# Kernel optimization log

Measured on AMD Instinct MI355X. Metric: run time of the kernel, lower is better.

## Reference

```python
import jax, jax.numpy as jnp
import numpy as np

PAD_MAG = 1e12
EPS = 1e-7  # matches prev_step.add_(1e-07) in the torch code


def setup_inputs() -> dict:
    key = jax.random.key(0)
    k1, k2, k3, k4 = jax.random.split(key, 4)
    B, txt_T, mel_T, n_mel = 16, 320, 2000, 80
    mu_logvar = jax.random.normal(k1, (B, txt_T, 2 * n_mel), dtype=jnp.float32)
    melspec = jax.random.normal(k2, (B, n_mel, mel_T), dtype=jnp.float32)
    text_lengths = jax.random.randint(k3, (B,), txt_T // 2, txt_T + 1).astype(jnp.int32)
    mel_lengths = jax.random.randint(k4, (B,), mel_T // 2, mel_T + 1).astype(jnp.int32)
    return {"mu_logvar": mu_logvar, "melspec": melspec,
            "text_lengths": text_lengths, "mel_lengths": mel_lengths}


def _log_prob_matrix(mu_logvar, melspec):
    # exponential[b,j,t] = -0.5 * mean_c( (x[b,t,c]-mu[b,j,c])^2 / exp(logvar) + logvar )
    # avoiding the [B,txt_T,mel_T,n_mel] broadcast the torch code materializes.
    n_mel = melspec.shape[1]
    mu = mu_logvar[:, :, :n_mel]          # [B, txt_T, n_mel]
    logvar = mu_logvar[:, :, n_mel:]      # [B, txt_T, n_mel]
    x = jnp.swapaxes(melspec, 1, 2)       # [B, mel_T, n_mel]
    inv_var = jnp.exp(-logvar)
    xx = jnp.einsum('btc,bjc->bjt', x * x, inv_var)
    xm = jnp.einsum('btc,bjc->bjt', x, mu * inv_var)
    mm = jnp.sum(mu * mu * inv_var + logvar, axis=2)  # [B, txt_T]
    return (-0.5 / n_mel) * (xx - 2.0 * xm + mm[:, :, None])  # [B, txt_T, mel_T]


def _forward_dp(log_prob, text_lengths, mel_lengths):
    # monotonic alignment forward algorithm (logsumexp DP over mel frames)
    B, txt_T, mel_T = log_prob.shape
    # carry = log_alpha column of size txt_T+1 (row 0 is the -inf pad row)
    init = jnp.full((B, txt_T + 1), -PAD_MAG, log_prob.dtype)
    init = init.at[:, 1].set(log_prob[:, 0, 0])

    def step(a, lp):  # a: [B, txt_T+1], lp: [B, txt_T]
        prev = jnp.stack([a[:, 1:], a[:, :-1]], axis=-1) + EPS
        tail = jax.nn.logsumexp(prev, axis=-1) + lp      # [B, txt_T]
        a_new = jnp.concatenate(
            [jnp.full((B, 1), -PAD_MAG, a.dtype), tail], axis=1)
        return a_new, tail

    lps = jnp.moveaxis(log_prob[:, :, 1:], 2, 0)         # [mel_T-1, B, txt_T]
    _, tails = jax.lax.scan(step, init, lps)             # [mel_T-1, B, txt_T]
    log_alpha = jnp.concatenate([init[None, :, 1:], tails], axis=0)  # [mel_T, B, txt_T]
    log_alpha = jnp.moveaxis(log_alpha, 0, 2)            # [B, txt_T, mel_T]

    bidx = jnp.arange(B)
    alpha_last = log_alpha[bidx, text_lengths - 1, mel_lengths - 1]
    alpha_last = alpha_last / mel_lengths.astype(log_alpha.dtype)
    return -jnp.mean(alpha_last)


def reference(mu_logvar, melspec, text_lengths, mel_lengths):
    log_prob = _log_prob_matrix(mu_logvar, melspec)
    mdn_loss = _forward_dp(log_prob, text_lengths, mel_lengths)
    return (mdn_loss, log_prob)
```

## Files before the change

kernel.cpp:

```cpp
#include <hip/hip_runtime.h>

#define BATCH 16
#define TXT   320
#define NMELC 80
#define MELT  2000
#define PADM  1.0e12f
#define EPSC  1e-7f
#define L2E   1.4426950408889634f
#define LN2   0.6931471805599453f
#define EPSL2 1.4426950e-7f

__global__ __launch_bounds__(256) void lp_kernel(
    const float* __restrict__ mlv,
    const float* __restrict__ ms,
    float* __restrict__ out_lp)
{
    __shared__ float Gt[16][64];
    __shared__ float Ft[16][256];
    __shared__ float bias_s[64];
    __shared__ float bias_p[256];

    const int b   = blockIdx.z;
    const int j0  = blockIdx.y * 64;
    const int t0  = blockIdx.x * 256;
    const int tid = threadIdx.x;
    const float s = -0.00625f;

    const float* mlv_b = mlv + (size_t)b * TXT * 160;
    const float* ms_b  = ms  + (size_t)b * NMELC * MELT;

    {
        const int jj = tid >> 2;
        const int q  = tid & 3;
        const float* p = mlv_b + (size_t)(j0 + jj) * 160 + q * 20;
        float part = 0.f;
        #pragma unroll
        for (int c = 0; c < 20; ++c) {
            float mu = p[c];
            float lv = p[c + 80];
            float iv = __expf(-lv);
            part += mu * mu * iv + lv;
        }
        bias_p[tid] = part;
    }
    __syncthreads();
    if (tid < 64) {
        float v = bias_p[tid * 4] + bias_p[tid * 4 + 1] +
                  bias_p[tid * 4 + 2] + bias_p[tid * 4 + 3];
        bias_s[tid] = s * v;
    }

    float acc[8][8];
    #pragma unroll
    for (int i = 0; i < 8; ++i)
        #pragma unroll
        for (int k = 0; k < 8; ++k) acc[i][k] = 0.f;

    const int jg = tid >> 5;
    const int tg = tid & 31;

    for (int kc = 0; kc < 10; ++kc) {
        const int c0 = kc * 8;
        __syncthreads();
        #pragma unroll
        for (int i = 0; i < 2; ++i) {
            int f   = tid + i * 256;
            int cr  = f >> 6;
            int col = f & 63;
            float mu = mlv_b[(size_t)(j0 + col) * 160 + (c0 + cr)];
            float lv = mlv_b[(size_t)(j0 + col) * 160 + (80 + c0 + cr)];
            float iv = __expf(-lv);
            Gt[cr][col]     = s * iv;
            Gt[cr + 8][col] = -2.f * s * mu * iv;
        }
        #pragma unroll
        for (int i = 0; i < 2; ++i) {
            int f   = tid + i * 256;
            int row = f >> 6;
            int c4  = f & 63;
            int t   = t0 + c4 * 4;
            float4 v = (t + 3 < MELT)
                ? *(const float4*)&ms_b[(size_t)(c0 + row) * MELT + t]
                : make_float4(0.f, 0.f, 0.f, 0.f);
            *(float4*)&Ft[row][c4 * 4] =
                make_float4(v.x * v.x, v.y * v.y, v.z * v.z, v.w * v.w);
            *(float4*)&Ft[row + 8][c4 * 4] = v;
        }
        __syncthreads();
        #pragma unroll
        for (int k = 0; k < 16; ++k) {
            float4 g0 = *(const float4*)&Gt[k][jg * 8];
            float4 g1 = *(const float4*)&Gt[k][jg * 8 + 4];
            float4 f0 = *(const float4*)&Ft[k][tg * 8];
            float4 f1 = *(const float4*)&Ft[k][tg * 8 + 4];
            float ga[8] = {g0.x, g0.y, g0.z, g0.w, g1.x, g1.y, g1.z, g1.w};
            float fa[8] = {f0.x, f0.y, f0.z, f0.w, f1.x, f1.y, f1.z, f1.w};
            #pragma unroll
            for (int ji = 0; ji < 8; ++ji)
                #pragma unroll
                for (int ti = 0; ti < 8; ++ti)
                    acc[ji][ti] = fmaf(ga[ji], fa[ti], acc[ji][ti]);
        }
    }

    #pragma unroll
    for (int ji = 0; ji < 8; ++ji) {
        int j = j0 + jg * 8 + ji;
        float bs = bias_s[jg * 8 + ji];
        float* orow = out_lp + (size_t)(b * TXT + j) * MELT;
        #pragma unroll
        for (int ti = 0; ti < 8; ++ti) {
            int t = t0 + tg * 8 + ti;
            if (t < MELT) orow[t] = acc[ji][ti] + bs;
        }
    }
}

__device__ __forceinline__ float dpp_shr1(float x) {
    return __int_as_float(__builtin_amdgcn_update_dpp(
        0, __float_as_int(x), 0x138 , 0xF, 0xF, false));
}

__global__ __launch_bounds__(192, 1) void dp_kernel(
    const float* __restrict__ lp,
    const int* __restrict__ tlen,
    const int* __restrict__ mlen,
    float* __restrict__ res,
    float* __restrict__ out0)
{
    __shared__ float bnd[2][2056];
    __shared__ int   prog[2];

    const int b    = blockIdx.x;
    const int tid  = threadIdx.x;
    const int w    = tid >> 6;
    const int l    = tid & 63;
    const int tend = mlen[b] - 1;
    const int tl   = tlen[b];

    if (tid < 2) prog[tid] = 0;

    int j0c = 2 * tid; if (j0c > 318) j0c = 318;
    const float* r0 = lp + (size_t)(b * TXT + j0c) * MELT;
    const float* r1 = r0 + MELT;

    float A1 = (tid == 0) ? lp[(size_t)b * TXT * MELT] * L2E : -PADM;
    float A2 = -PADM;
    float A1F = A1, A2F = A2;

    if (l == 63 && w < 2) bnd[w][0] = -PADM;
    __syncthreads();

    if (w == 2 && tl < 257) return;

    float ptA2 = -PADM, ptB2 = -PADM;
    const bool is0     = (l == 0);
    const bool isPub   = (l == 63) && (w < 2);
    const bool hasRing = (w > 0);
    int seen = 0;

    const int imax = tend + 63;

    float PA[16], PB[16], PC[16];
    #pragma unroll
    for (int q = 0; q < 8; ++q) { PA[2*q] = r0[1 + q - l]; PA[2*q+1] = r1[1 + q - l]; }
    #pragma unroll
    for (int q = 0; q < 8; ++q) { PB[2*q] = r0[9 + q - l]; PB[2*q+1] = r1[9 + q - l]; }
    #pragma unroll
    for (int q = 0; q < 16; ++q) PA[q] = fmaf(PA[q], L2E, EPSL2);

    const float* p0 = r0 + 17 - l;
    const float* p1 = r1 + 17 - l;

#define RING_RD(BQ_, T0_)                                                    \
    {                                                                        \
        float4 r0_ = *(const float4*)&bnd[w - 1][T0_];                       \
        float4 r1_ = *(const float4*)&bnd[w - 1][(T0_) + 4];                 \
        BQ_[0]=r0_.x; BQ_[1]=r0_.y; BQ_[2]=r0_.z; BQ_[3]=r0_.w;              \
        BQ_[4]=r1_.x; BQ_[5]=r1_.y; BQ_[6]=r1_.z; BQ_[7]=r1_.w;              \
    }
#define RING_POLL(NEED_)                                                     \
    if (seen < (NEED_)) {                                                    \
        int tgt_ = (NEED_) + 32;                                             \
        if (tgt_ > tend - 1) tgt_ = tend - 1;                                \
        if (tgt_ < (NEED_)) tgt_ = (NEED_);                                  \
        volatile int* pv_ = &prog[w - 1];                                    \
        int v_ = *pv_;                                                       \
        while (v_ < tgt_) { __builtin_amdgcn_s_sleep(1); v_ = *pv_; }        \
        seen = v_;                                                           \
        __asm__ volatile("" ::: "memory");                                   \
    }

    float bqC[8];
    if (hasRing) {
        RING_POLL(7)
        RING_RD(bqC, 0)
    } else {
        #pragma unroll
        for (int q = 0; q < 8; ++q) bqC[q] = -PADM;
    }

#define STEP2(Pc_, q_, AQ_)                                                  \
    {                                                                        \
        float pt_ = is0 ? bqC[q_] : ptA2;                                    \
        float m1_ = fmaxf(A1, pt_);                                          \
        float d1_ = A1 - pt_;                                                \
        float e1_ = __builtin_amdgcn_exp2f(-fabsf(d1_));                     \
        float g1_ = __builtin_amdgcn_logf(1.0f + e1_);                       \
        float n1_ = m1_ + g1_ + Pc_[2 * q_];                                 \
        float m2_ = fmaxf(A2, A1);                                           \
        float d2_ = A2 - A1;                                                 \
        float e2_ = __builtin_amdgcn_exp2f(-fabsf(d2_));                     \
        float g2_ = __builtin_amdgcn_logf(1.0f + e2_);                       \
        float n2_ = m2_ + g2_ + Pc_[2 * q_ + 1];                             \
        float ns_ = dpp_shr1(n2_);                                           \
        ptA2 = ptB2; ptB2 = ns_;                                             \
        A1 = n1_; A2 = n2_; AQ_ = n2_;                                       \
    }

#define GROUP2_S(Pc_, Pm_, Pl_, I0_)                                         \
{                                                                            \
    float bqN[8];                                                            \
    if (hasRing) {                                                           \
        const int nt0_ = (I0_) + 7;                                          \
        RING_POLL(nt0_ + 7)                                                  \
        RING_RD(bqN, nt0_)                                                   \
    } else {                                                                 \
        _Pragma("unroll") for (int q_=0;q_<8;++q_) bqN[q_] = -PADM;          \
    }                                                                        \
    _Pragma("unroll") for (int q_=0;q_<8;++q_) {                             \
        Pl_[2*q_] = p0[q_]; Pl_[2*q_+1] = p1[q_];                            \
    }                                                                        \
    float aq2[8];                                                            \
    _Pragma("unroll")                                                        \
    for (int q_=0;q_<8;++q_) STEP2(Pc_, q_, aq2[q_])                         \
    if (isPub) {                                                             \
        const int t63_ = (I0_) - 63;                                         \
        if (t63_ >= 1) {                                                     \
            _Pragma("unroll") for (int q_=0;q_<8;++q_)                       \
                bnd[w][t63_ + q_] = aq2[q_];                                 \
        } else {                                                             \
            _Pragma("unroll") for (int q_=0;q_<8;++q_)                       \
                if (t63_ + q_ >= 1) bnd[w][t63_ + q_] = aq2[q_];             \
        }                                                                    \
        __asm__ volatile("" ::: "memory");          \
        int pgv_ = t63_ + 7;                                                 \
        if (pgv_ >= 1) prog[w] = pgv_;                                       \
    }                                                                        \
    p0 += 8; p1 += 8;                                                        \
    _Pragma("unroll") for (int q_=0;q_<16;++q_)                              \
        Pm_[q_] = fmaf(Pm_[q_], L2E, EPSL2);                                 \
    _Pragma("unroll") for (int q_=0;q_<8;++q_) bqC[q_] = bqN[q_];            \
}

#define GROUP2_T(Pc_, Pm_, Pl_, I0_)                                         \
{                                                                            \
    float bqN[8];                                                            \
    if (hasRing) {                                                           \
        const int nt0_ = (I0_) + 7;                                          \
        int need_ = nt0_ + 7; if (need_ > tend - 1) need_ = tend - 1;        \
        RING_POLL(need_)                                                     \
        const int rb_ = nt0_ > 2048 ? 2048 : nt0_;                           \
        RING_RD(bqN, rb_)                                                    \
    } else {                                                                 \
        _Pragma("unroll") for (int q_=0;q_<8;++q_) bqN[q_] = -PADM;          \
    }                                                                        \
    _Pragma("unroll") for (int q_=0;q_<8;++q_) {                             \
        int t_ = (I0_) + 16 + q_ - l;                                        \
        t_ = t_ < 0 ? 0 : (t_ > tend ? tend : t_);                           \
        Pl_[2*q_] = r0[t_]; Pl_[2*q_+1] = r1[t_];                            \
    }                                                                        \
    float aq2[8];                                                            \
    const int vt_ = (I0_) - l;                                               \
    _Pragma("unroll")                                                        \
    for (int q_=0;q_<8;++q_) {                                               \
        STEP2(Pc_, q_, aq2[q_])                                              \
        bool c_ = (vt_ + q_ == tend);                                        \
        A1F = c_ ? A1 : A1F;                                                 \
        A2F = c_ ? A2 : A2F;                                                 \
    }                                                                        \
    if (isPub) {                                                             \
        const int t63_ = (I0_) - 63;                                         \
        _Pragma("unroll") for (int q_=0;q_<8;++q_) {                         \
            int tq_ = t63_ + q_;                                             \
            if (tq_ >= 1 && tq_ <= tend) bnd[w][tq_] = aq2[q_];              \
        }                                                                    \
        __asm__ volatile("" ::: "memory");                                   \
        int pgv_ = t63_ + 7; if (pgv_ > tend) pgv_ = tend;                   \
        if (pgv_ >= 1) prog[w] = pgv_;                                       \
    }                                                                        \
    _Pragma("unroll") for (int q_=0;q_<16;++q_)                              \
        Pm_[q_] = fmaf(Pm_[q_], L2E, EPSL2);                                 \
    _Pragma("unroll") for (int q_=0;q_<8;++q_) bqC[q_] = bqN[q_];            \
}

    int i0 = 1;
    const int sEnd = tend - 23;
    int ph = 0;
    while (i0 <= sEnd) {
        GROUP2_S(PA, PB, PC, i0); i0 += 8;
        if (i0 > sEnd) { ph = 1; break; }
        GROUP2_S(PB, PC, PA, i0); i0 += 8;
        if (i0 > sEnd) { ph = 2; break; }
        GROUP2_S(PC, PA, PB, i0); i0 += 8;
    }
    if (ph == 1) {
        #pragma unroll
        for (int q = 0; q < 16; ++q) {
            float tmp = PA[q]; PA[q] = PB[q]; PB[q] = PC[q]; PC[q] = tmp;
        }
    } else if (ph == 2) {
        #pragma unroll
        for (int q = 0; q < 16; ++q) {
            float tmp = PA[q]; PA[q] = PC[q]; PC[q] = PB[q]; PB[q] = tmp;
        }
    }
    while (i0 <= imax) {
        GROUP2_T(PA, PB, PC, i0); i0 += 8;
        if (i0 > imax) break;
        GROUP2_T(PB, PC, PA, i0); i0 += 8;
        if (i0 > imax) break;
        GROUP2_T(PC, PA, PB, i0); i0 += 8;
    }

#undef GROUP2_S
#undef GROUP2_T
#undef STEP2
#undef RING_RD
#undef RING_POLL

    if (tid == ((tl - 1) >> 1)) {
        float Af = ((tl - 1) & 1) ? A2F : A1F;
        float v = Af * LN2 / (float)(tend + 1);
        if (res) res[b] = v;
        else     atomicAdd(out0, -v / (float)BATCH);
    }
}

__global__ void zero1_kernel(float* out0) { out0[0] = 0.f; }

__global__ void fin_kernel(const float* __restrict__ res, float* __restrict__ out0)
{
    int l = threadIdx.x;
    float v = (l < BATCH) ? res[l] : 0.f;
    #pragma unroll
    for (int off = 32; off; off >>= 1) v += __shfl_down(v, off);
    if (l == 0) out0[0] = -(v / (float)BATCH);
}

extern "C" void kernel_launch(void* const* d_in, const int* in_sizes, int n_in,
                              void* d_out, int out_size, void* d_ws, size_t ws_size,
                              hipStream_t stream)
{
    const float* mlv = (const float*)d_in[0];
    const float* ms  = (const float*)d_in[1];
    const int*   tl  = (const int*)d_in[2];
    const int*   ml  = (const int*)d_in[3];
    float* out    = (float*)d_out;
    float* out_lp = out + 1;

    bool res_ok = ws_size >= 64;
    float* res = res_ok ? (float*)d_ws : nullptr;

    dim3 gA(8, 5, 16);
    lp_kernel<<<gA, 256, 0, stream>>>(mlv, ms, out_lp);

    if (!res_ok) zero1_kernel<<<1, 1, 0, stream>>>(out);
    dp_kernel<<<BATCH, 192, 0, stream>>>(out_lp, tl, ml, res, out);
    if (res_ok) fin_kernel<<<1, 64, 0, stream>>>(res, out);
}
```

Baseline: 244.7 us.

## Precompute 4-step DP transition coefficients in parallel kernel, then run strided wavefront DP

New measurement: 937.8 us. 283% more time.

```diff
diff --git a/kernel.cpp b/kernel.cpp
--- a/kernel.cpp
+++ b/kernel.cpp
@@ -4,7 +4,9 @@
 #define TXT   320
 #define NMELC 80
 #define MELT  2000
+#define NW    504
 #define PADM  1.0e12f
+#define INF9  1.0e9f
 #define EPSC  1e-7f
 #define L2E   1.4426950408889634f
 #define LN2   0.6931471805599453f
@@ -116,12 +118,264 @@
     }
 }
 
+__device__ __forceinline__ float lse2l(float x, float y) {
+    float m = fmaxf(x, y);
+    float d = x - y;
+    float e = __builtin_amdgcn_exp2f(-fabsf(d));
+    return m + __builtin_amdgcn_logf(1.0f + e);
+}
+
+__global__ __launch_bounds__(320) void coeff_kernel(
+    const float* __restrict__ lp,
+    const int* __restrict__ mlen,
+    float* __restrict__ Cc)
+{
+    __shared__ float sl[320][65];
+
+    const int Wg  = blockIdx.x;
+    const int b   = blockIdx.y;
+    const int tid = threadIdx.x;
+    const int tend = mlen[b] - 1;
+
+    {
+        const int g  = tid >> 6;
+        const int tl_ = tid & 63;
+        const int t  = 64 * Wg + 1 + tl_;
+        for (int r = 0; r < 64; ++r) {
+            int j = g * 64 + r;
+            float v = (t < MELT) ? lp[((size_t)b * TXT + j) * MELT + t] : 0.f;
+            sl[j][tl_] = fmaf(v, L2E, EPSL2);
+        }
+    }
+    __syncthreads();
+
+    const int j = tid;
+    const int j1 = j >= 1 ? j - 1 : 0;
+    const int j2 = j >= 2 ? j - 2 : 0;
+    const int j3 = j >= 3 ? j - 3 : 0;
+
+    for (int wi = 0; wi < 16; ++wi) {
+        const int W = Wg * 16 + wi;
+        if (W >= NW) break;
+        const int col = 4 * wi;
+
+        float B0[5] = {0.f, -INF9, -INF9, -INF9, -INF9};
+        float B1[5] = {0.f, -INF9, -INF9, -INF9, -INF9};
+        float B2[5] = {0.f, -INF9, -INF9, -INF9, -INF9};
+        float B3[5] = {0.f, -INF9, -INF9, -INF9, -INF9};
+
+        if (4 * W + 1 <= tend) {
+            float p0 = sl[j][col], p1 = sl[j1][col], p2 = sl[j2][col], p3 = sl[j3][col];
+            B3[1] = p3 + lse2l(B3[1], 0.f);      B3[0] = p3 + B3[0];
+            B2[1] = p2 + lse2l(B2[1], B3[0] - p3);
+        }
+        {
+            float O0[5], O1[5], O2[5], O3[5];
+            #pragma unroll
+            for (int r = 0; r < 5; ++r) { O0[r]=0.f; O1[r]=0.f; O2[r]=0.f; O3[r]=0.f; }
+            #pragma unroll
+            for (int r = 0; r < 5; ++r) {
+                B0[r] = r==0?0.f:-INF9; B1[r] = r==0?0.f:-INF9;
+                B2[r] = r==0?0.f:-INF9; B3[r] = r==0?0.f:-INF9;
+            }
+            if (4 * W + 1 <= tend) {
+                float p0 = sl[j][col], p1 = sl[j1][col], p2 = sl[j2][col], p3 = sl[j3][col];
+                #pragma unroll
+                for (int r = 0; r < 5; ++r) { O0[r]=B0[r]; O1[r]=B1[r]; O2[r]=B2[r]; O3[r]=B3[r]; }
+                B0[0] = p0 + O0[0];  B0[1] = p0 + lse2l(O0[1], O1[0]);
+                B1[0] = p1 + O1[0];  B1[1] = p1 + lse2l(O1[1], O2[0]);
+                B2[0] = p2 + O2[0];  B2[1] = p2 + lse2l(O2[1], O3[0]);
+                B3[0] = p3 + O3[0];  B3[1] = p3 + lse2l(O3[1], 0.f);
+            }
+            if (4 * W + 2 <= tend) {
+                float p0 = sl[j][col+1], p1 = sl[j1][col+1], p2 = sl[j2][col+1];
+                #pragma unroll
+                for (int r = 0; r < 5; ++r) { O0[r]=B0[r]; O1[r]=B1[r]; O2[r]=B2[r]; O3[r]=B3[r]; }
+                B0[0] = p0 + O0[0];
+                B0[1] = p0 + lse2l(O0[1], O1[0]);
+                B0[2] = p0 + lse2l(O0[2], O1[1]);
+                B1[0] = p1 + O1[0];
+                B1[1] = p1 + lse2l(O1[1], O2[0]);
+                B1[2] = p1 + lse2l(O1[2], O2[1]);
+                B2[0] = p2 + O2[0];
+                B2[1] = p2 + lse2l(O2[1], O3[0]);
+                B2[2] = p2 + lse2l(O2[2], O3[1]);
+            }
+            if (4 * W + 3 <= tend) {
+                float p0 = sl[j][col+2], p1 = sl[j1][col+2];
+                #pragma unroll
+                for (int r = 0; r < 5; ++r) { O0[r]=B0[r]; O1[r]=B1[r]; O2[r]=B2[r]; }
+                B0[0] = p0 + O0[0];
+                B0[1] = p0 + lse2l(O0[1], O1[0]);
+                B0[2] = p0 + lse2l(O0[2], O1[1]);
+                B0[3] = p0 + lse2l(O0[3], O1[2]);
+                B1[0] = p1 + O1[0];
+                B1[1] = p1 + lse2l(O1[1], O2[0]);
+                B1[2] = p1 + lse2l(O1[2], O2[1]);
+                B1[3] = p1 + lse2l(O1[3], O2[2]);
+            }
+            if (4 * W + 4 <= tend) {
+                float p0 = sl[j][col+3];
+                #pragma unroll
+                for (int r = 0; r < 5; ++r) { O0[r]=B0[r]; O1[r]=B1[r]; }
+                B0[0] = p0 + O0[0];
+                B0[1] = p0 + lse2l(O0[1], O1[0]);
+                B0[2] = p0 + lse2l(O0[2], O1[1]);
+                B0[3] = p0 + lse2l(O0[3], O1[2]);
+                B0[4] = p0 + lse2l(O0[4], O1[3]);
+            }
+        }
+        if (j < 1) B0[1] = -INF9;
+        if (j < 2) B0[2] = -INF9;
+        if (j < 3) B0[3] = -INF9;
+        if (j < 4) B0[4] = -INF9;
+
+        float* cp = Cc + (((size_t)b * NW + W) * 5) * 320 + j;
+        cp[0]    = B0[0];
+        cp[320]  = B0[1];
+        cp[640]  = B0[2];
+        cp[960]  = B0[3];
+        cp[1280] = B0[4];
+    }
+}
+
 __device__ __forceinline__ float dpp_shr1(float x) {
     return __int_as_float(__builtin_amdgcn_update_dpp(
         0, __float_as_int(x), 0x138 , 0xF, 0xF, false));
 }
 
-__global__ __launch_bounds__(192, 1) void dp_kernel(
+__global__ __launch_bounds__(320, 1) void dp_kernel(
+    const float* __restrict__ Cc,
+    const float* __restrict__ lp,
+    const int* __restrict__ tlen,
+    const int* __restrict__ mlen,
+    float* __restrict__ res,
+    float* __restrict__ out0)
+{
+    __shared__ float bnd[4][NW][4];
+    __shared__ int   prog[4];
+
+    const int b    = blockIdx.x;
+    const int tid  = threadIdx.x;
+    const int w    = tid >> 6;
+    const int l    = tid & 63;
+    const int j    = tid;
+    const int tend = mlen[b] - 1;
+    const int tl   = tlen[b];
+    const int Wmax = (tend + 3) >> 2;
+
+    if (tid < 4) prog[tid] = 0;
+
+    float a  = (j == 0) ? lp[(size_t)b * TXT * MELT] * L2E : -PADM;
+    float aF = a;
+    if (l >= 60 && w < 4) bnd[w][0][l - 60] = a;
+    __syncthreads();
+
+    float H1 = -PADM, H2 = -PADM, H3 = -PADM, H4 = -PADM;
+    const bool hasRing = (w > 0);
+    int seen = -1;
+    const float* Cb = Cc + ((size_t)b * NW * 5) * 320 + j;
+    const int imax = Wmax - 1 + 63;
+
+    float CA[4][5], CB[4][5];
+    float RA[4][4], RB[4][4];
+    #pragma unroll
+    for (int q = 0; q < 4; ++q)
+        #pragma unroll
+        for (int k = 0; k < 4; ++k) { RA[q][k] = -PADM; RB[q][k] = -PADM; }
+
+#define CLAMPW(I_, OUT_) { int W_ = (I_) - l; W_ = W_ < 0 ? 0 : W_;          \
+    OUT_ = W_ > Wmax - 1 ? Wmax - 1 : W_; }
+
+#define POLLTO(TGT_) if (hasRing) {                                          \
+    int need_ = (TGT_); if (need_ > Wmax - 1) need_ = Wmax - 1;              \
+    if (seen < need_) {                                                      \
+        int t2_ = need_ + 16; if (t2_ > Wmax - 1) t2_ = Wmax - 1;            \
+        volatile int* pv_ = &prog[w - 1];                                    \
+        int v_ = *pv_;                                                       \
+        while (v_ < t2_) { __builtin_amdgcn_s_sleep(1); v_ = *pv_; }         \
+        seen = v_;                                                           \
+        __asm__ volatile("" ::: "memory");                                   \
+    } }
+
+#define LOADG(CX_, RX_, IB_) {                                               \
+    _Pragma("unroll")                                                        \
+    for (int q_ = 0; q_ < 4; ++q_) {                                         \
+        int We_; CLAMPW((IB_) + q_, We_)                                     \
+        const float* cp_ = Cb + (size_t)We_ * 1600;                          \
+        CX_[q_][0] = cp_[0];    CX_[q_][1] = cp_[320];                       \
+        CX_[q_][2] = cp_[640];  CX_[q_][3] = cp_[960];                       \
+        CX_[q_][4] = cp_[1280];                                              \
+        if (hasRing) {                                                       \
+            if (l < 1) RX_[q_][0] = bnd[w - 1][We_][3];                      \
+            if (l < 2) RX_[q_][1] = bnd[w - 1][We_][l + 2];                  \
+            if (l < 3) RX_[q_][2] = bnd[w - 1][We_][l + 1];                  \
+            if (l < 4) RX_[q_][3] = bnd[w - 1][We_][l];                      \
+        }                                                                    \
+    } }
+
+#define STEP(CQ_, RQ_, I_) {                                                 \
+    H4 = dpp_shr1(H3); H3 = dpp_shr1(H2); H2 = dpp_shr1(H1);                 \
+    H1 = dpp_shr1(a);                                                        \
+    float N1_ = (l >= 1) ? H1 : RQ_[0];                                      \
+    float N2_ = (l >= 2) ? H2 : RQ_[1];                                      \
+    float N3_ = (l >= 3) ? H3 : RQ_[2];                                      \
+    float N4_ = (l >= 4) ? H4 : RQ_[3];                                      \
+    float x0_ = a   + CQ_[0];                                                \
+    float x1_ = N1_ + CQ_[1];                                                \
+    float x2_ = N2_ + CQ_[2];                                                \
+    float x3_ = N3_ + CQ_[3];                                                \
+    float x4_ = N4_ + CQ_[4];                                                \
+    float m_ = fmaxf(fmaxf(fmaxf(x0_, x1_), fmaxf(x2_, x3_)), x4_);          \
+    float s_ = __builtin_amdgcn_exp2f(x0_ - m_)                              \
+             + __builtin_amdgcn_exp2f(x1_ - m_)                              \
+             + __builtin_amdgcn_exp2f(x2_ - m_)                              \
+             + __builtin_amdgcn_exp2f(x3_ - m_)                              \
+             + __builtin_amdgcn_exp2f(x4_ - m_);                             \
+    a = m_ + __builtin_amdgcn_logf(s_);                                      \
+    aF = ((I_) - l == Wmax - 1) ? a : aF;                                    \
+    if (l >= 60 && w < 4) {                                                  \
+        int Wp_ = (I_) - l + 1;                                              \
+        if (Wp_ >= 1 && Wp_ <= Wmax - 1) bnd[w][Wp_][l - 60] = a;            \
+    } }
+
+#define PHASE(CC_, RC_, CN_, RN_, I0_) {                                     \
+    POLLTO((I0_) + 7)                                                        \
+    LOADG(CN_, RN_, (I0_) + 4)                                               \
+    STEP(CC_[0], RC_[0], (I0_) + 0)                                          \
+    STEP(CC_[1], RC_[1], (I0_) + 1)                                          \
+    STEP(CC_[2], RC_[2], (I0_) + 2)                                          \
+    STEP(CC_[3], RC_[3], (I0_) + 3)                                          \
+    if (l == 63 && w < 4) {                                                  \
+        __asm__ volatile("s_waitcnt lgkmcnt(0)" ::: "memory");               \
+        int pv_ = (I0_) + 3 - 62;                                            \
+        if (pv_ > Wmax - 1) pv_ = Wmax - 1;                                  \
+        if (pv_ >= 0) prog[w] = pv_;                                         \
+    } }
+
+    POLLTO(3)
+    LOADG(CA, RA, 0)
+
+    int i0 = 0;
+    while (true) {
+        PHASE(CA, RA, CB, RB, i0); i0 += 4; if (i0 > imax) break;
+        PHASE(CB, RB, CA, RA, i0); i0 += 4; if (i0 > imax) break;
+    }
+
+#undef PHASE
+#undef STEP
+#undef LOADG
+#undef POLLTO
+#undef CLAMPW
+
+    if (tid == tl - 1) {
+        float v = aF * LN2 / (float)(tend + 1);
+        if (res) res[b] = v;
+        else     atomicAdd(out0, -v / (float)BATCH);
+    }
+}
+
+__global__ __launch_bounds__(192, 1) void dp_kernel_fb(
     const float* __restrict__ lp,
     const int* __restrict__ tlen,
     const int* __restrict__ mlen,
@@ -174,10 +428,10 @@
 
 #define RING_RD(BQ_, T0_)                                                    \
     {                                                                        \
-        float4 r0_ = *(const float4*)&bnd[w - 1][T0_];                       \
-        float4 r1_ = *(const float4*)&bnd[w - 1][(T0_) + 4];                 \
-        BQ_[0]=r0_.x; BQ_[1]=r0_.y; BQ_[2]=r0_.z; BQ_[3]=r0_.w;              \
-        BQ_[4]=r1_.x; BQ_[5]=r1_.y; BQ_[6]=r1_.z; BQ_[7]=r1_.w;              \
+        float4 q0_ = *(const float4*)&bnd[w - 1][T0_];                       \
+        float4 q1_ = *(const float4*)&bnd[w - 1][(T0_) + 4];                 \
+        BQ_[0]=q0_.x; BQ_[1]=q0_.y; BQ_[2]=q0_.z; BQ_[3]=q0_.w;              \
+        BQ_[4]=q1_.x; BQ_[5]=q1_.y; BQ_[6]=q1_.z; BQ_[7]=q1_.w;              \
     }
 #define RING_POLL(NEED_)                                                     \
     if (seen < (NEED_)) {                                                    \
@@ -243,7 +497,7 @@
             _Pragma("unroll") for (int q_=0;q_<8;++q_)                       \
                 if (t63_ + q_ >= 1) bnd[w][t63_ + q_] = aq2[q_];             \
         }                                                                    \
-        __asm__ volatile("" ::: "memory");          \
+        __asm__ volatile("" ::: "memory");                                   \
         int pgv_ = t63_ + 7;                                                 \
         if (pgv_ >= 1) prog[w] = pgv_;                                       \
     }                                                                        \
@@ -359,13 +613,21 @@
     float* out    = (float*)d_out;
     float* out_lp = out + 1;
 
+    const size_t C_bytes = (size_t)BATCH * NW * 5 * 320 * sizeof(float);
     bool res_ok = ws_size >= 64;
+    bool has_C  = ws_size >= 64 + C_bytes;
     float* res = res_ok ? (float*)d_ws : nullptr;
+    float* Cc  = has_C ? (float*)((char*)d_ws + 64) : nullptr;
 
     dim3 gA(8, 5, 16);
     lp_kernel<<<gA, 256, 0, stream>>>(mlv, ms, out_lp);
 
     if (!res_ok) zero1_kernel<<<1, 1, 0, stream>>>(out);
-    dp_kernel<<<BATCH, 192, 0, stream>>>(out_lp, tl, ml, res, out);
+    if (has_C) {
+        coeff_kernel<<<dim3(32, 16), 320, 0, stream>>>(out_lp, ml, Cc);
+        dp_kernel<<<BATCH, 320, 0, stream>>>(Cc, out_lp, tl, ml, res, out);
+    } else {
+        dp_kernel_fb<<<BATCH, 192, 0, stream>>>(out_lp, tl, ml, res, out);
+    }
     if (res_ok) fin_kernel<<<1, 64, 0, stream>>>(res, out);
 }
```

## Pre-skew log_prob into diagonal-major layout for the wavefront DP

Applied to the files above, without the earlier changes.

Result: slower. 258.4 us (+5.6%).

```diff
diff --git a/kernel.cpp b/kernel.cpp
--- a/kernel.cpp
+++ b/kernel.cpp
@@ -4,6 +4,7 @@
 #define TXT   320
 #define NMELC 80
 #define MELT  2000
+#define DIAGS 2240
 #define PADM  1.0e12f
 #define EPSC  1e-7f
 #define L2E   1.4426950408889634f
@@ -116,13 +117,46 @@
     }
 }
 
+__global__ __launch_bounds__(256) void tr_kernel(
+    const float* __restrict__ lp,
+    float* __restrict__ lpS)
+{
+    __shared__ float T[64][65];
+    const int b    = blockIdx.z;
+    const int j0   = blockIdx.y * 64;
+    const int t0   = blockIdx.x * 64;
+    const int tid  = threadIdx.x;
+    const int lane = tid & 63;
+    const int qg   = tid >> 6;
+
+    #pragma unroll 4
+    for (int it = 0; it < 16; ++it) {
+        int j = j0 + qg * 16 + it;
+        int t = t0 + lane;
+        float v = (t < MELT) ? lp[((size_t)b * TXT + j) * MELT + t] : 0.f;
+        T[qg * 16 + it][lane] = fmaf(v, L2E, EPSL2);
+    }
+    __syncthreads();
+
+    const int rbase = t0 + (j0 >> 1);
+    float* orow = lpS + ((size_t)b * DIAGS + rbase) * TXT + j0 + lane;
+    #pragma unroll 4
+    for (int k = 0; k < 24; ++k) {
+        int d = qg + 4 * k;
+        if (d > 94) break;
+        int tloc = d - (lane >> 1);
+        if (tloc >= 0 && tloc < 64 && (t0 + tloc) < MELT)
+            orow[(size_t)d * TXT] = T[lane][tloc];
+    }
+}
+
 __device__ __forceinline__ float dpp_shr1(float x) {
     return __int_as_float(__builtin_amdgcn_update_dpp(
         0, __float_as_int(x), 0x138 , 0xF, 0xF, false));
 }
 
 __global__ __launch_bounds__(192, 1) void dp_kernel(
-    const float* __restrict__ lp,
+    const float* __restrict__ lpS,
     const int* __restrict__ tlen,
     const int* __restrict__ mlen,
     float* __restrict__ res,
@@ -140,11 +174,10 @@
 
     if (tid < 2) prog[tid] = 0;
 
-    int j0c = 2 * tid; if (j0c > 318) j0c = 318;
-    const float* r0 = lp + (size_t)(b * TXT + j0c) * MELT;
-    const float* r1 = r0 + MELT;
-
-    float A1 = (tid == 0) ? lp[(size_t)b * TXT * MELT] * L2E : -PADM;
+    const float* rowp = lpS + (size_t)b * DIAGS * TXT
+                      + (size_t)(64 * w) * TXT + 2 * tid;
+
+    float A1 = (tid == 0) ? rowp[0] - EPSL2 : -PADM;
     float A2 = -PADM;
     float A1F = A1, A2F = A2;
 
@@ -163,14 +196,16 @@
 
     float PA[16], PB[16], PC[16];
     #pragma unroll
-    for (int q = 0; q < 8; ++q) { PA[2*q] = r0[1 + q - l]; PA[2*q+1] = r1[1 + q - l]; }
-    #pragma unroll
-    for (int q = 0; q < 8; ++q) { PB[2*q] = r0[9 + q - l]; PB[2*q+1] = r1[9 + q - l]; }
-    #pragma unroll
-    for (int q = 0; q < 16; ++q) PA[q] = fmaf(PA[q], L2E, EPSL2);
-
-    const float* p0 = r0 + 17 - l;
-    const float* p1 = r1 + 17 - l;
+    for (int q = 0; q < 8; ++q) {
+        float2 v = *(const float2*)&rowp[(size_t)(1 + q) * TXT];
+        PA[2 * q] = v.x; PA[2 * q + 1] = v.y;
+    }
+    #pragma unroll
+    for (int q = 0; q < 8; ++q) {
+        float2 v = *(const float2*)&rowp[(size_t)(9 + q) * TXT];
+        PB[2 * q] = v.x; PB[2 * q + 1] = v.y;
+    }
+    const float* pref = rowp + (size_t)17 * TXT;
 
 #define RING_RD(BQ_, T0_)                                                    \
     {                                                                        \
@@ -218,7 +253,7 @@
         A1 = n1_; A2 = n2_; AQ_ = n2_;                                       \
     }
 
-#define GROUP2_S(Pc_, Pm_, Pl_, I0_)                                         \
+#define GROUP2_S(Pc_, Pl_, I0_)                                              \
 {                                                                            \
     float bqN[8];                                                            \
     if (hasRing) {                                                           \
@@ -229,7 +264,8 @@
         _Pragma("unroll") for (int q_=0;q_<8;++q_) bqN[q_] = -PADM;          \
     }                                                                        \
     _Pragma("unroll") for (int q_=0;q_<8;++q_) {                             \
-        Pl_[2*q_] = p0[q_]; Pl_[2*q_+1] = p1[q_];                            \
+        float2 v_ = *(const float2*)&pref[(size_t)q_ * TXT];                 \
+        Pl_[2*q_] = v_.x; Pl_[2*q_+1] = v_.y;                                \
     }                                                                        \
     float aq2[8];                                                            \
     _Pragma("unroll")                                                        \
@@ -247,6 +283,219 @@
         int pgv_ = t63_ + 7;                                                 \
         if (pgv_ >= 1) prog[w] = pgv_;                                       \
     }                                                                        \
+    pref += (size_t)8 * TXT;                                                 \
+    _Pragma("unroll") for (int q_=0;q_<8;++q_) bqC[q_] = bqN[q_];            \
+}
+
+#define GROUP2_T(Pc_, Pl_, I0_)                                              \
+{                                                                            \
+    float bqN[8];                                                            \
+    if (hasRing) {                                                           \
+        const int nt0_ = (I0_) + 7;                                          \
+        int need_ = nt0_ + 7; if (need_ > tend - 1) need_ = tend - 1;        \
+        RING_POLL(need_)                                                     \
+        const int rb_ = nt0_ > 2048 ? 2048 : nt0_;                           \
+        RING_RD(bqN, rb_)                                                    \
+    } else {                                                                 \
+        _Pragma("unroll") for (int q_=0;q_<8;++q_) bqN[q_] = -PADM;          \
+    }                                                                        \
+    _Pragma("unroll") for (int q_=0;q_<8;++q_) {                             \
+        float2 v_ = *(const float2*)&pref[(size_t)q_ * TXT];                 \
+        Pl_[2*q_] = v_.x; Pl_[2*q_+1] = v_.y;                                \
+    }                                                                        \
+    float aq2[8];                                                            \
+    const int vt_ = (I0_) - l;                                               \
+    _Pragma("unroll")                                                        \
+    for (int q_=0;q_<8;++q_) {                                               \
+        STEP2(Pc_, q_, aq2[q_])                                              \
+        bool c_ = (vt_ + q_ == tend);                                        \
+        A1F = c_ ? A1 : A1F;                                                 \
+        A2F = c_ ? A2 : A2F;                                                 \
+    }                                                                        \
+    if (isPub) {                                                             \
+        const int t63_ = (I0_) - 63;                                         \
+        _Pragma("unroll") for (int q_=0;q_<8;++q_) {                         \
+            int tq_ = t63_ + q_;                                             \
+            if (tq_ >= 1 && tq_ <= tend) bnd[w][tq_] = aq2[q_];              \
+        }                                                                    \
+        __asm__ volatile("" ::: "memory");                                   \
+        int pgv_ = t63_ + 7; if (pgv_ > tend) pgv_ = tend;                   \
+        if (pgv_ >= 1) prog[w] = pgv_;                                       \
+    }                                                                        \
+    pref += (size_t)8 * TXT;                                                 \
+    _Pragma("unroll") for (int q_=0;q_<8;++q_) bqC[q_] = bqN[q_];            \
+}
+
+    int i0 = 1;
+    const int sEnd = tend - 23;
+    int ph = 0;
+    while (i0 <= sEnd) {
+        GROUP2_S(PA, PC, i0); i0 += 8;
+        if (i0 > sEnd) { ph = 1; break; }
+        GROUP2_S(PB, PA, i0); i0 += 8;
+        if (i0 > sEnd) { ph = 2; break; }
+        GROUP2_S(PC, PB, i0); i0 += 8;
+    }
+    if (ph == 1) {
+        #pragma unroll
+        for (int q = 0; q < 16; ++q) {
+            float tmp = PA[q]; PA[q] = PB[q]; PB[q] = PC[q]; PC[q] = tmp;
+        }
+    } else if (ph == 2) {
+        #pragma unroll
+        for (int q = 0; q < 16; ++q) {
+            float tmp = PA[q]; PA[q] = PC[q]; PC[q] = PB[q]; PB[q] = tmp;
+        }
+    }
+    while (i0 <= imax) {
+        GROUP2_T(PA, PC, i0); i0 += 8;
+        if (i0 > imax) break;
+        GROUP2_T(PB, PA, i0); i0 += 8;
+        if (i0 > imax) break;
+        GROUP2_T(PC, PB, i0); i0 += 8;
+    }
+
+#undef GROUP2_S
+#undef GROUP2_T
+#undef STEP2
+#undef RING_RD
+#undef RING_POLL
+
+    if (tid == ((tl - 1) >> 1)) {
+        float Af = ((tl - 1) & 1) ? A2F : A1F;
+        float v = Af * LN2 / (float)(tend + 1);
+        if (res) res[b] = v;
+        else     atomicAdd(out0, -v / (float)BATCH);
+    }
+}
+
+__global__ __launch_bounds__(192, 1) void dp_kernel_fb(
+    const float* __restrict__ lp,
+    const int* __restrict__ tlen,
+    const int* __restrict__ mlen,
+    float* __restrict__ res,
+    float* __restrict__ out0)
+{
+    __shared__ float bnd[2][2056];
+    __shared__ int   prog[2];
+
+    const int b    = blockIdx.x;
+    const int tid  = threadIdx.x;
+    const int w    = tid >> 6;
+    const int l    = tid & 63;
+    const int tend = mlen[b] - 1;
+    const int tl   = tlen[b];
+
+    if (tid < 2) prog[tid] = 0;
+
+    int j0c = 2 * tid; if (j0c > 318) j0c = 318;
+    const float* r0 = lp + (size_t)(b * TXT + j0c) * MELT;
+    const float* r1 = r0 + MELT;
+
+    float A1 = (tid == 0) ? lp[(size_t)b * TXT * MELT] * L2E : -PADM;
+    float A2 = -PADM;
+    float A1F = A1, A2F = A2;
+
+    if (l == 63 && w < 2) bnd[w][0] = -PADM;
+    __syncthreads();
+
+    if (w == 2 && tl < 257) return;
+
+    float ptA2 = -PADM, ptB2 = -PADM;
+    const bool is0     = (l == 0);
+    const bool isPub   = (l == 63) && (w < 2);
+    const bool hasRing = (w > 0);
+    int seen = 0;
+
+    const int imax = tend + 63;
+
+    float PA[16], PB[16], PC[16];
+    #pragma unroll
+    for (int q = 0; q < 8; ++q) { PA[2*q] = r0[1 + q - l]; PA[2*q+1] = r1[1 + q - l]; }
+    #pragma unroll
+    for (int q = 0; q < 8; ++q) { PB[2*q] = r0[9 + q - l]; PB[2*q+1] = r1[9 + q - l]; }
+    #pragma unroll
+    for (int q = 0; q < 16; ++q) PA[q] = fmaf(PA[q], L2E, EPSL2);
+
+    const float* p0 = r0 + 17 - l;
+    const float* p1 = r1 + 17 - l;
+
+#define RING_RD(BQ_, T0_)                                                    \
+    {                                                                        \
+        float4 q0_ = *(const float4*)&bnd[w - 1][T0_];                       \
+        float4 q1_ = *(const float4*)&bnd[w - 1][(T0_) + 4];                 \
+        BQ_[0]=q0_.x; BQ_[1]=q0_.y; BQ_[2]=q0_.z; BQ_[3]=q0_.w;              \
+        BQ_[4]=q1_.x; BQ_[5]=q1_.y; BQ_[6]=q1_.z; BQ_[7]=q1_.w;              \
+    }
+#define RING_POLL(NEED_)                                                     \
+    if (seen < (NEED_)) {                                                    \
+        int tgt_ = (NEED_) + 32;                                             \
+        if (tgt_ > tend - 1) tgt_ = tend - 1;                                \
+        if (tgt_ < (NEED_)) tgt_ = (NEED_);                                  \
+        volatile int* pv_ = &prog[w - 1];                                    \
+        int v_ = *pv_;                                                       \
+        while (v_ < tgt_) { __builtin_amdgcn_s_sleep(1); v_ = *pv_; }        \
+        seen = v_;                                                           \
+        __asm__ volatile("" ::: "memory");                                   \
+    }
+
+    float bqC[8];
+    if (hasRing) {
+        RING_POLL(7)
+        RING_RD(bqC, 0)
+    } else {
+        #pragma unroll
+        for (int q = 0; q < 8; ++q) bqC[q] = -PADM;
+    }
+
+#define STEP2(Pc_, q_, AQ_)                                                  \
+    {                                                                        \
+        float pt_ = is0 ? bqC[q_] : ptA2;                                    \
+        float m1_ = fmaxf(A1, pt_);                                          \
+        float d1_ = A1 - pt_;                                                \
+        float e1_ = __builtin_amdgcn_exp2f(-fabsf(d1_));                     \
+        float g1_ = __builtin_amdgcn_logf(1.0f + e1_);                       \
+        float n1_ = m1_ + g1_ + Pc_[2 * q_];                                 \
+        float m2_ = fmaxf(A2, A1);                                           \
+        float d2_ = A2 - A1;                                                 \
+        float e2_ = __builtin_amdgcn_exp2f(-fabsf(d2_));                     \
+        float g2_ = __builtin_amdgcn_logf(1.0f + e2_);                       \
+        float n2_ = m2_ + g2_ + Pc_[2 * q_ + 1];                             \
+        float ns_ = __int_as_float(__builtin_amdgcn_update_dpp(              \
+            0, __float_as_int(n2_), 0x138, 0xF, 0xF, false));                \
+        ptA2 = ptB2; ptB2 = ns_;                                             \
+        A1 = n1_; A2 = n2_; AQ_ = n2_;                                       \
+    }
+
+#define GROUP2_S(Pc_, Pm_, Pl_, I0_)                                         \
+{                                                                            \
+    float bqN[8];                                                            \
+    if (hasRing) {                                                           \
+        const int nt0_ = (I0_) + 7;                                          \
+        RING_POLL(nt0_ + 7)                                                  \
+        RING_RD(bqN, nt0_)                                                   \
+    } else {                                                                 \
+        _Pragma("unroll") for (int q_=0;q_<8;++q_) bqN[q_] = -PADM;          \
+    }                                                                        \
+    _Pragma("unroll") for (int q_=0;q_<8;++q_) {                             \
+        Pl_[2*q_] = p0[q_]; Pl_[2*q_+1] = p1[q_];                            \
+    }                                                                        \
+    float aq2[8];                                                            \
+    _Pragma("unroll")                                                        \
+    for (int q_=0;q_<8;++q_) STEP2(Pc_, q_, aq2[q_])                         \
+    if (isPub) {                                                             \
+        const int t63_ = (I0_) - 63;                                         \
+        if (t63_ >= 1) {                                                     \
+            _Pragma("unroll") for (int q_=0;q_<8;++q_)                       \
+                bnd[w][t63_ + q_] = aq2[q_];                                 \
+        } else {                                                             \
+            _Pragma("unroll") for (int q_=0;q_<8;++q_)                       \
+                if (t63_ + q_ >= 1) bnd[w][t63_ + q_] = aq2[q_];             \
+        }                                                                    \
+        __asm__ volatile("" ::: "memory");                                   \
+        int pgv_ = t63_ + 7;                                                 \
+        if (pgv_ >= 1) prog[w] = pgv_;                                       \
+    }                                                                        \
     p0 += 8; p1 += 8;                                                        \
     _Pragma("unroll") for (int q_=0;q_<16;++q_)                              \
         Pm_[q_] = fmaf(Pm_[q_], L2E, EPSL2);                                 \
@@ -359,13 +608,21 @@
     float* out    = (float*)d_out;
     float* out_lp = out + 1;
 
-    bool res_ok = ws_size >= 64;
+    const size_t lpS_bytes = (size_t)BATCH * DIAGS * TXT * sizeof(float);
+    bool res_ok = ws_size >= 128;
+    bool has_S  = ws_size >= 128 + lpS_bytes;
     float* res = res_ok ? (float*)d_ws : nullptr;
+    float* lpS = has_S ? (float*)((char*)d_ws + 128) : nullptr;
 
     dim3 gA(8, 5, 16);
     lp_kernel<<<gA, 256, 0, stream>>>(mlv, ms, out_lp);
 
     if (!res_ok) zero1_kernel<<<1, 1, 0, stream>>>(out);
-    dp_kernel<<<BATCH, 192, 0, stream>>>(out_lp, tl, ml, res, out);
+    if (has_S) {
+        tr_kernel<<<dim3(32, 5, 16), 256, 0, stream>>>(out_lp, lpS);
+        dp_kernel<<<BATCH, 192, 0, stream>>>(lpS, tl, ml, res, out);
+    } else {
+        dp_kernel_fb<<<BATCH, 192, 0, stream>>>(out_lp, tl, ml, res, out);
+    }
     if (res_ok) fin_kernel<<<1, 64, 0, stream>>>(res, out);
 }
```

## Fuse log-prob GEMM and DP into one kernel with per-chunk readiness flags

Applied to the files above, without the earlier changes.

Result: no change. 243.7 us (-0.4%).

```diff
diff --git a/kernel.cpp b/kernel.cpp
--- a/kernel.cpp
+++ b/kernel.cpp
@@ -5,24 +5,19 @@
 #define NMELC 80
 #define MELT  2000
 #define PADM  1.0e12f
-#define EPSC  1e-7f
 #define L2E   1.4426950408889634f
 #define LN2   0.6931471805599453f
 #define EPSL2 1.4426950e-7f
 
-__global__ __launch_bounds__(256) void lp_kernel(
-    const float* __restrict__ mlv,
-    const float* __restrict__ ms,
-    float* __restrict__ out_lp)
-{
-    __shared__ float Gt[16][64];
-    __shared__ float Ft[16][256];
-    __shared__ float bias_s[64];
-    __shared__ float bias_p[256];
-
-    const int b   = blockIdx.z;
-    const int j0  = blockIdx.y * 64;
-    const int t0  = blockIdx.x * 256;
+__device__ __forceinline__ void lp_block(
+    const float* __restrict__ mlv, const float* __restrict__ ms,
+    float* __restrict__ out_lp, int b, int j0, int t0, float* SM)
+{
+    float (*Gt)[64]  = (float(*)[64])SM;
+    float (*Ft)[256] = (float(*)[256])(SM + 1024);
+    float* bias_p    = SM + 5120;
+    float* bias_s    = SM + 5376;
+
     const int tid = threadIdx.x;
     const float s = -0.00625f;
 
@@ -116,22 +111,14 @@
     }
 }
 
-__device__ __forceinline__ float dpp_shr1(float x) {
-    return __int_as_float(__builtin_amdgcn_update_dpp(
-        0, __float_as_int(x), 0x138 , 0xF, 0xF, false));
-}
-
-__global__ __launch_bounds__(192, 1) void dp_kernel(
-    const float* __restrict__ lp,
-    const int* __restrict__ tlen,
-    const int* __restrict__ mlen,
-    float* __restrict__ res,
-    float* __restrict__ out0)
-{
-    __shared__ float bnd[2][2056];
-    __shared__ int   prog[2];
-
-    const int b    = blockIdx.x;
+__device__ __forceinline__ void dp_block(
+    const float* __restrict__ lp, const int* __restrict__ tlen,
+    const int* __restrict__ mlen, float* __restrict__ res,
+    float* __restrict__ out0, int b, float* SM, int* flags)
+{
+    float (*bnd)[2056] = (float(*)[2056])SM;
+    int* prog = (int*)(SM + 4112);
+
     const int tid  = threadIdx.x;
     const int w    = tid >> 6;
     const int l    = tid & 63;
@@ -139,6 +126,17 @@
     const int tl   = tlen[b];
 
     if (tid < 2) prog[tid] = 0;
+    if (l == 63 && w < 2) bnd[w][0] = -PADM;
+    __syncthreads();
+    if (tid >= 192) return;
+
+#define CHUNK_WAIT(C_)                                                       \
+    while (__hip_atomic_load(&flags[(b << 3) + (C_)], __ATOMIC_ACQUIRE,      \
+                             __HIP_MEMORY_SCOPE_AGENT) < 5)                  \
+        __builtin_amdgcn_s_sleep(8);
+
+    int lastC = 0;
+    if (flags) { CHUNK_WAIT(0) }
 
     int j0c = 2 * tid; if (j0c > 318) j0c = 318;
     const float* r0 = lp + (size_t)(b * TXT + j0c) * MELT;
@@ -147,9 +145,6 @@
     float A1 = (tid == 0) ? lp[(size_t)b * TXT * MELT] * L2E : -PADM;
     float A2 = -PADM;
     float A1F = A1, A2F = A2;
-
-    if (l == 63 && w < 2) bnd[w][0] = -PADM;
-    __syncthreads();
 
     if (w == 2 && tl < 257) return;
 
@@ -174,10 +169,10 @@
 
 #define RING_RD(BQ_, T0_)                                                    \
     {                                                                        \
-        float4 r0_ = *(const float4*)&bnd[w - 1][T0_];                       \
-        float4 r1_ = *(const float4*)&bnd[w - 1][(T0_) + 4];                 \
-        BQ_[0]=r0_.x; BQ_[1]=r0_.y; BQ_[2]=r0_.z; BQ_[3]=r0_.w;              \
-        BQ_[4]=r1_.x; BQ_[5]=r1_.y; BQ_[6]=r1_.z; BQ_[7]=r1_.w;              \
+        float4 q0_ = *(const float4*)&bnd[w - 1][T0_];                       \
+        float4 q1_ = *(const float4*)&bnd[w - 1][(T0_) + 4];                 \
+        BQ_[0]=q0_.x; BQ_[1]=q0_.y; BQ_[2]=q0_.z; BQ_[3]=q0_.w;              \
+        BQ_[4]=q1_.x; BQ_[5]=q1_.y; BQ_[6]=q1_.z; BQ_[7]=q1_.w;              \
     }
 #define RING_POLL(NEED_)                                                     \
     if (seen < (NEED_)) {                                                    \
@@ -189,6 +184,11 @@
         while (v_ < tgt_) { __builtin_amdgcn_s_sleep(1); v_ = *pv_; }        \
         seen = v_;                                                           \
         __asm__ volatile("" ::: "memory");                                   \
+    }
+#define CHUNK_STEP(I0_)                                                      \
+    if (flags) {                                                             \
+        int cN_ = ((I0_) + 31) >> 8; if (cN_ > 7) cN_ = 7;                   \
+        while (lastC < cN_) { ++lastC; CHUNK_WAIT(lastC) }                   \
     }
 
     float bqC[8];
@@ -213,13 +213,15 @@
         float e2_ = __builtin_amdgcn_exp2f(-fabsf(d2_));                     \
         float g2_ = __builtin_amdgcn_logf(1.0f + e2_);                       \
         float n2_ = m2_ + g2_ + Pc_[2 * q_ + 1];                             \
-        float ns_ = dpp_shr1(n2_);                                           \
+        float ns_ = __int_as_float(__builtin_amdgcn_update_dpp(              \
+            0, __float_as_int(n2_), 0x138, 0xF, 0xF, false));                \
         ptA2 = ptB2; ptB2 = ns_;                                             \
         A1 = n1_; A2 = n2_; AQ_ = n2_;                                       \
     }
 
 #define GROUP2_S(Pc_, Pm_, Pl_, I0_)                                         \
 {                                                                            \
+    CHUNK_STEP(I0_)                                                          \
     float bqN[8];                                                            \
     if (hasRing) {                                                           \
         const int nt0_ = (I0_) + 7;                                          \
@@ -243,7 +245,7 @@
             _Pragma("unroll") for (int q_=0;q_<8;++q_)                       \
                 if (t63_ + q_ >= 1) bnd[w][t63_ + q_] = aq2[q_];             \
         }                                                                    \
-        __asm__ volatile("" ::: "memory");          \
+        __asm__ volatile("" ::: "memory");                                   \
         int pgv_ = t63_ + 7;                                                 \
         if (pgv_ >= 1) prog[w] = pgv_;                                       \
     }                                                                        \
@@ -255,6 +257,7 @@
 
 #define GROUP2_T(Pc_, Pm_, Pl_, I0_)                                         \
 {                                                                            \
+    CHUNK_STEP(I0_)                                                          \
     float bqN[8];                                                            \
     if (hasRing) {                                                           \
         const int nt0_ = (I0_) + 7;                                          \
@@ -328,6 +331,8 @@
 #undef STEP2
 #undef RING_RD
 #undef RING_POLL
+#undef CHUNK_STEP
+#undef CHUNK_WAIT
 
     if (tid == ((tl - 1) >> 1)) {
         float Af = ((tl - 1) & 1) ? A2F : A1F;
@@ -337,7 +342,52 @@
     }
 }
 
-__global__ void zero1_kernel(float* out0) { out0[0] = 0.f; }
+__global__ __launch_bounds__(256) void fused_kernel(
+    const float* __restrict__ mlv, const float* __restrict__ ms,
+    float* __restrict__ out_lp,
+    const int* __restrict__ tlen, const int* __restrict__ mlen,
+    float* __restrict__ res, int* __restrict__ flags)
+{
+    __shared__ float SM[5440];
+    const int blk = blockIdx.x;
+    if (blk < BATCH) {
+        dp_block(out_lp, tlen, mlen, res, nullptr, blk, SM, flags);
+        return;
+    }
+    const int r  = blk - BATCH;
+    const int tc = r / 80;
+    const int rem = r % 80;
+    const int b  = rem / 5;
+    const int jt = rem % 5;
+    lp_block(mlv, ms, out_lp, b, jt * 64, tc * 256, SM);
+    __syncthreads();
+    if (threadIdx.x == 0)
+        __hip_atomic_fetch_add(&flags[(b << 3) + tc], 1,
+                               __ATOMIC_RELEASE, __HIP_MEMORY_SCOPE_AGENT);
+}
+
+__global__ __launch_bounds__(256) void lp_kernel(
+    const float* __restrict__ mlv, const float* __restrict__ ms,
+    float* __restrict__ out_lp)
+{
+    __shared__ float SM[5440];
+    lp_block(mlv, ms, out_lp, blockIdx.z, blockIdx.y * 64, blockIdx.x * 256, SM);
+}
+
+__global__ __launch_bounds__(256) void dp_kernel_fb(
+    const float* __restrict__ lp, const int* __restrict__ tlen,
+    const int* __restrict__ mlen, float* __restrict__ res,
+    float* __restrict__ out0)
+{
+    __shared__ float SM[5440];
+    dp_block(lp, tlen, mlen, res, out0, blockIdx.x, SM, nullptr);
+}
+
+__global__ void init_kernel(int* flags, float* out0, int zero_out)
+{
+    if (threadIdx.x < 128) flags[threadIdx.x] = 0;
+    if (threadIdx.x == 0 && zero_out) out0[0] = 0.f;
+}
 
 __global__ void fin_kernel(const float* __restrict__ res, float* __restrict__ out0)
 {
@@ -359,13 +409,21 @@
     float* out    = (float*)d_out;
     float* out_lp = out + 1;
 
-    bool res_ok = ws_size >= 64;
-    float* res = res_ok ? (float*)d_ws : nullptr;
-
-    dim3 gA(8, 5, 16);
-    lp_kernel<<<gA, 256, 0, stream>>>(mlv, ms, out_lp);
-
-    if (!res_ok) zero1_kernel<<<1, 1, 0, stream>>>(out);
-    dp_kernel<<<BATCH, 192, 0, stream>>>(out_lp, tl, ml, res, out);
-    if (res_ok) fin_kernel<<<1, 64, 0, stream>>>(res, out);
-}
+    bool res_ok   = ws_size >= 64;
+    bool fused_ok = ws_size >= 64 + 512;
+    float* res  = res_ok ? (float*)d_ws : nullptr;
+    int*  flags = fused_ok ? (int*)((char*)d_ws + 64) : nullptr;
+
+    if (fused_ok) {
+        init_kernel<<<1, 128, 0, stream>>>(flags, out, 0);
+        fused_kernel<<<BATCH + 8 * 5 * BATCH, 256, 0, stream>>>(
+            mlv, ms, out_lp, tl, ml, res, flags);
+        fin_kernel<<<1, 64, 0, stream>>>(res, out);
+    } else {
+        dim3 gA(8, 5, 16);
+        lp_kernel<<<gA, 256, 0, stream>>>(mlv, ms, out_lp);
+        if (!res_ok) init_kernel<<<1, 1, 0, stream>>>((int*)d_ws, out, 1);
+        dp_kernel_fb<<<BATCH, 256, 0, stream>>>(out_lp, tl, ml, res, out);
+        if (res_ok) fin_kernel<<<1, 64, 0, stream>>>(res, out);
+    }
+}
```
